# Performance work log

Hardware: AMD Instinct MI355X
Metric: run time of the kernel (lower is better)

## Reference

```python
import jax, jax.numpy as jnp
import numpy as np

VOCAB, EMB, HID, OUT = 50257, 512, 1024, 5
SEQ, BATCH = 512, 64


def setup_inputs() -> dict:
    key = jax.random.key(0)
    ks = jax.random.split(key, 8)
    s_e = 1.0
    s_ih = 1.0 / np.sqrt(HID)
    return {
        "text": jax.random.randint(ks[0], (SEQ, BATCH), 0, VOCAB, dtype=jnp.int32),
        "emb": jax.random.normal(ks[1], (VOCAB, EMB), dtype=jnp.float32) * s_e,
        "W_ih": jax.random.normal(ks[2], (EMB, 3 * HID), dtype=jnp.float32) * s_ih,
        "W_hh": jax.random.normal(ks[3], (HID, 3 * HID), dtype=jnp.float32) * s_ih,
        "b_ih": jax.random.normal(ks[4], (3 * HID,), dtype=jnp.float32) * s_ih,
        "b_hh": jax.random.normal(ks[5], (3 * HID,), dtype=jnp.float32) * s_ih,
        "fc_W": jax.random.normal(ks[6], (HID, OUT), dtype=jnp.float32) * s_ih,
        "fc_b": jnp.zeros((OUT,), dtype=jnp.float32),
    }


def _gru_step(h, x_t, W_ih, W_hh, b_ih, b_hh):
    # Standard GRU cell (torch.nn.GRUCell math):
    # r = sigmoid(x Wir + bir + h Whr + bhr)
    # z = sigmoid(x Wiz + biz + h Whz + bhz)
    # h' = (1 - z) * n + z * h
    gi = x_t @ W_ih + b_ih              # [B, 3H]
    gh = h @ W_hh + b_hh                # [B, 3H]
    i_r, i_z, i_n = jnp.split(gi, 3, axis=-1)
    h_r, h_z, h_n = jnp.split(gh, 3, axis=-1)
    r = jax.nn.sigmoid(i_r + h_r)
    z = jax.nn.sigmoid(i_z + h_z)
    n = jnp.tanh(i_n + r * h_n)
    return (1.0 - z) * n + z * h


def reference(text, emb, W_ih, W_hh, b_ih, b_hh, fc_W, fc_b):
    embedded = emb[text]                # [S, B, E]
    h0 = jnp.zeros((embedded.shape[1], HID), dtype=embedded.dtype)

    def step(h, x_t):
        h_new = _gru_step(h, x_t, W_ih, W_hh, b_ih, b_hh)
        return h_new, None

    h_final, _ = jax.lax.scan(step, h0, embedded)
    return h_final @ fc_W + fc_b        # [B, OUT]
```

## Files before the change

kernel.cpp:

```cpp
#include <hip/hip_runtime.h>
#include <hip/hip_cooperative_groups.h>
#include <hip/hip_bf16.h>
#include <math.h>

constexpr int EMBD  = 512;
constexpr int HID   = 1024;
constexpr int NOUT  = 5;
constexpr int SEQ   = 512;
constexpr int BATCH = 64;

constexpr int NBLK = 64;
constexpr int NTHR = 512;
constexpr int JPB  = 16;

typedef __attribute__((ext_vector_type(8))) short bf16x8;
typedef __attribute__((ext_vector_type(4))) float f32x4;

__device__ inline unsigned short f2bf(float f) {
    __hip_bfloat16 h = __float2bfloat16(f);
    return *reinterpret_cast<unsigned short*>(&h);
}

__device__ inline bf16x8 cvt8v(f32x4 a, f32x4 b) {
    bf16x8 r;
#pragma unroll
    for (int i = 0; i < 4; i++) { __hip_bfloat16 h = __float2bfloat16(a[i]); r[i]     = *reinterpret_cast<short*>(&h); }
#pragma unroll
    for (int i = 0; i < 4; i++) { __hip_bfloat16 h = __float2bfloat16(b[i]); r[4 + i] = *reinterpret_cast<short*>(&h); }
    return r;
}

__device__ inline unsigned long long load_a8(const unsigned short* p) {
    return __hip_atomic_load((const unsigned long long*)p,
                             __ATOMIC_RELAXED, __HIP_MEMORY_SCOPE_AGENT);
}
__device__ inline void store_a8(unsigned short* p, unsigned long long v) {
    __hip_atomic_store((unsigned long long*)p, v,
                       __ATOMIC_RELAXED, __HIP_MEMORY_SCOPE_AGENT);
}
__device__ inline bf16x8 load_frag(const unsigned short* p) {
    union { unsigned long long u[2]; bf16x8 v; } r;
    r.u[0] = load_a8(p);
    r.u[1] = load_a8(p + 4);
    return r.v;
}

__device__ inline float sigm(float x) { return 1.f / (1.f + __expf(-x)); }
__device__ inline float ftanh(float x) { return 1.f - 2.f / (1.f + __expf(2.f * x)); }

__global__ __launch_bounds__(256) void pack_w(const float* __restrict__ W,
                                              unsigned short* __restrict__ out,
                                              int K) {
    const int nkt = K / 32;
    long idx = (long)blockIdx.x * 256 + threadIdx.x;
    const long total = (long)NBLK * 3 * nkt * 64;
    if (idx >= total) return;
    const int lane = idx & 63;
    long rest = idx >> 6;
    const int kt = rest % nkt; rest /= nkt;
    const int nt = rest % 3;
    const int g  = rest / 3;
    const int k0  = kt * 32 + (lane >> 4) * 8;
    const int col = nt * HID + g * JPB + (lane & 15);
    unsigned short* o = out + idx * 8;
#pragma unroll
    for (int i = 0; i < 8; i++)
        o[i] = f2bf(W[(long)(k0 + i) * 3072 + col]);
}

__global__ __launch_bounds__(256) void embed_x(const int* __restrict__ text,
                                               const float* __restrict__ emb,
                                               unsigned short* __restrict__ xfrag) {
    long idx = (long)blockIdx.x * 256 + threadIdx.x;
    if (idx >= (long)SEQ * 4 * 16 * 64) return;
    const int lane = idx & 63;
    const int kt   = (idx >> 6) & 15;
    const int bt   = (idx >> 10) & 3;
    const int t    = (int)(idx >> 12);
    const int b    = bt * 16 + (lane & 15);
    const int e0   = kt * 32 + (lane >> 4) * 8;
    const int tok  = text[t * BATCH + b];
    const float* s = emb + (long)tok * EMBD + e0;
    *(bf16x8*)(xfrag + idx * 8) = cvt8v(*(const f32x4*)s, *(const f32x4*)(s + 4));
}

__global__ void __launch_bounds__(NTHR, 2) gru_mfma(
    const unsigned short* __restrict__ xfrag,
    const float*          __restrict__ b_ih,
    const float*          __restrict__ b_hh,
    const float*          __restrict__ fc_W,
    const float*          __restrict__ fc_b,
    const unsigned short* __restrict__ whh_f,
    const unsigned short* __restrict__ wih_f,
    unsigned short*       __restrict__ hbuf,
    int*                  __restrict__ flags,
    float*                __restrict__ out)
{
    const int g    = blockIdx.x;
    const int tid  = threadIdx.x;
    const int lane = tid & 63;
    const int w    = tid >> 6;
    const int mp   = w >> 2;
    const int kq   = w & 3;
    const int l16  = lane & 15;
    const int lhi  = lane >> 4;

    __shared__ float red[8][8][256];
    __shared__ unsigned short hx[64][20];

    constexpr int HFRAG = 4 * 32 * 64 * 8;

    for (int i = tid; i < 512; i += NTHR)
        store_a8(hbuf + ((long)g * 512 + i) * 4, 0ull);

    const int jg = g * JPB + l16;
    const float bir  = b_ih[jg],           bhr = b_hh[jg];
    const float biz  = b_ih[HID + jg],     bhz = b_hh[HID + jg];
    const float bin_ = b_ih[2 * HID + jg], bhn = b_hh[2 * HID + jg];

    const bool gateW  = (kq < 2);
    const bool storeW = (kq >= 2);
    const int  mtG    = mp * 2 + kq;
    const int  mtS    = mp * 2 + (kq - 2);
    float hp[4] = {0.f, 0.f, 0.f, 0.f};

    bf16x8 xa0[4], xa1[4];
    auto loadX = [&](int t) {
        const unsigned short* base = xfrag + (long)t * (4 * 16 * 64 * 8);
#pragma unroll
        for (int kk = 0; kk < 4; kk++) {
            const int kt = kq * 4 + kk;
            xa0[kk] = load_frag(base + (((2 * mp + 0) * 16 + kt) * 64 + lane) * 8);
            xa1[kk] = load_frag(base + (((2 * mp + 1) * 16 + kt) * 64 + lane) * 8);
        }
    };

    const int sb  = mtS * 16 + ((lane >> 1) & 15);
    const int sjl = ((lane >> 1) >> 4) * 8 + 4 * (lane & 1);
    const long sdst = (((long)mtS * 32 + (g >> 1)) * 64) * 8 + 256 * (g & 1) + lane * 4;

    const unsigned short* whh_g = whh_f + (long)g * 3 * 32 * 64 * 8;
    const unsigned short* wih_g = wih_f + (long)g * 3 * 16 * 64 * 8;

    asm volatile("s_waitcnt vmcnt(0)" ::: "memory");
    __syncthreads();
    if (tid == 0)
        __hip_atomic_store(&flags[g], 1, __ATOMIC_RELAXED, __HIP_MEMORY_SCOPE_AGENT);
    loadX(0);
    if (tid < 64) {
        int f = __hip_atomic_load(&flags[tid], __ATOMIC_RELAXED, __HIP_MEMORY_SCOPE_AGENT);
        while (__any(f < 1)) {
            __builtin_amdgcn_s_sleep(1);
            f = __hip_atomic_load(&flags[tid], __ATOMIC_RELAXED, __HIP_MEMORY_SCOPE_AGENT);
        }
    }
    __syncthreads();

    for (int t = 0; t < SEQ; ++t) {
        const unsigned short* hr = hbuf + (long)(t & 1) * HFRAG;
        unsigned short*       hw = hbuf + (long)((t + 1) & 1) * HFRAG;

        bf16x8 ha0[8], ha1[8];
#pragma unroll
        for (int kk = 0; kk < 8; kk++) {
            const int kt = kq * 8 + kk;
            ha0[kk] = load_frag(hr + (((long)(2 * mp + 0) * 32 + kt) * 64 + lane) * 8);
            ha1[kk] = load_frag(hr + (((long)(2 * mp + 1) * 32 + kt) * 64 + lane) * 8);
        }

        f32x4 aR0 = {0,0,0,0}, aR1 = {0,0,0,0};
        f32x4 aZ0 = {0,0,0,0}, aZ1 = {0,0,0,0};
        f32x4 aGh0 = {0,0,0,0}, aGh1 = {0,0,0,0};
        f32x4 aGi0 = {0,0,0,0}, aGi1 = {0,0,0,0};

#pragma unroll
        for (int kk = 0; kk < 4; kk++) {
            const unsigned short* bp = wih_g + (((long)(kq * 4 + kk)) * 64 + lane) * 8;
            const bf16x8 bR = *(const bf16x8*)(bp);
            const bf16x8 bZ = *(const bf16x8*)(bp + 16 * 64 * 8);
            const bf16x8 bN = *(const bf16x8*)(bp + 2 * 16 * 64 * 8);
            aR0  = __builtin_amdgcn_mfma_f32_16x16x32_bf16(xa0[kk], bR, aR0, 0, 0, 0);
            aR1  = __builtin_amdgcn_mfma_f32_16x16x32_bf16(xa1[kk], bR, aR1, 0, 0, 0);
            aZ0  = __builtin_amdgcn_mfma_f32_16x16x32_bf16(xa0[kk], bZ, aZ0, 0, 0, 0);
            aZ1  = __builtin_amdgcn_mfma_f32_16x16x32_bf16(xa1[kk], bZ, aZ1, 0, 0, 0);
            aGi0 = __builtin_amdgcn_mfma_f32_16x16x32_bf16(xa0[kk], bN, aGi0, 0, 0, 0);
            aGi1 = __builtin_amdgcn_mfma_f32_16x16x32_bf16(xa1[kk], bN, aGi1, 0, 0, 0);
        }

#pragma unroll
        for (int kk = 0; kk < 8; kk++) {
            const int kt = kq * 8 + kk;
            const unsigned short* bp = whh_g + (((long)kt) * 64 + lane) * 8;
            const bf16x8 bR = *(const bf16x8*)(bp);
            const bf16x8 bZ = *(const bf16x8*)(bp + 32 * 64 * 8);
            const bf16x8 bN = *(const bf16x8*)(bp + 2 * 32 * 64 * 8);
            aR0  = __builtin_amdgcn_mfma_f32_16x16x32_bf16(ha0[kk], bR, aR0, 0, 0, 0);
            aR1  = __builtin_amdgcn_mfma_f32_16x16x32_bf16(ha1[kk], bR, aR1, 0, 0, 0);
            aZ0  = __builtin_amdgcn_mfma_f32_16x16x32_bf16(ha0[kk], bZ, aZ0, 0, 0, 0);
            aZ1  = __builtin_amdgcn_mfma_f32_16x16x32_bf16(ha1[kk], bZ, aZ1, 0, 0, 0);
            aGh0 = __builtin_amdgcn_mfma_f32_16x16x32_bf16(ha0[kk], bN, aGh0, 0, 0, 0);
            aGh1 = __builtin_amdgcn_mfma_f32_16x16x32_bf16(ha1[kk], bN, aGh1, 0, 0, 0);
        }

        *(f32x4*)&red[w][0][lane * 4] = aR0;
        *(f32x4*)&red[w][1][lane * 4] = aR1;
        *(f32x4*)&red[w][2][lane * 4] = aZ0;
        *(f32x4*)&red[w][3][lane * 4] = aZ1;
        *(f32x4*)&red[w][4][lane * 4] = aGh0;
        *(f32x4*)&red[w][5][lane * 4] = aGh1;
        *(f32x4*)&red[w][6][lane * 4] = aGi0;
        *(f32x4*)&red[w][7][lane * 4] = aGi1;
        __syncthreads();

        if (gateW) {
            const int s = kq;
            f32x4 R  = {0,0,0,0}, Z = {0,0,0,0}, Gh = {0,0,0,0}, Gi = {0,0,0,0};
#pragma unroll
            for (int q = 0; q < 4; q++) {
                const int src = mp * 4 + q;
                R  += *(const f32x4*)&red[src][0 + s][lane * 4];
                Z  += *(const f32x4*)&red[src][2 + s][lane * 4];
                Gh += *(const f32x4*)&red[src][4 + s][lane * 4];
                Gi += *(const f32x4*)&red[src][6 + s][lane * 4];
            }
#pragma unroll
            for (int r = 0; r < 4; r++) {
                const float rr = sigm(R[r] + bir + bhr);
                const float zz = sigm(Z[r] + biz + bhz);
                const float nn = ftanh(Gi[r] + bin_ + rr * (Gh[r] + bhn));
                const float hn = (1.f - zz) * nn + zz * hp[r];
                hp[r] = hn;
                hx[mtG * 16 + lhi * 4 + r][l16] = f2bf(hn);
            }
        }
        __syncthreads();

        if (storeW) {
            const unsigned long long v =
                *(const unsigned long long*)&hx[sb][sjl];
            store_a8(hw + sdst, v);
            asm volatile("s_waitcnt vmcnt(0)" ::: "memory");
        }
        __syncthreads();

        if (tid == 0)
            __hip_atomic_store(&flags[g], t + 2, __ATOMIC_RELAXED, __HIP_MEMORY_SCOPE_AGENT);
        loadX((t + 1 < SEQ) ? t + 1 : SEQ - 1);
        if (tid < 64) {
            int f = __hip_atomic_load(&flags[tid], __ATOMIC_RELAXED, __HIP_MEMORY_SCOPE_AGENT);
            while (__any(f < t + 2)) {
                __builtin_amdgcn_s_sleep(1);
                f = __hip_atomic_load(&flags[tid], __ATOMIC_RELAXED, __HIP_MEMORY_SCOPE_AGENT);
            }
        }
        __syncthreads();
    }

    float (*hsl)[JPB] = reinterpret_cast<float(*)[JPB]>(&red[0][0][0]);
    if (gateW) {
#pragma unroll
        for (int r = 0; r < 4; r++) {
            const int b = mtG * 16 + lhi * 4 + r;
            hsl[b][l16] = hp[r];
        }
    }
    __syncthreads();
    if (tid < BATCH * NOUT) {
        const int b = tid / NOUT, o = tid - b * NOUT;
        float acc = (g == 0) ? fc_b[o] : 0.0f;
#pragma unroll
        for (int jl = 0; jl < JPB; jl++)
            acc += hsl[b][jl] * fc_W[(g * JPB + jl) * NOUT + o];
        atomicAdd(&out[tid], acc);
    }
}

extern "C" void kernel_launch(void* const* d_in, const int* in_sizes, int n_in,
                              void* d_out, int out_size, void* d_ws, size_t ws_size,
                              hipStream_t stream) {
    const int*   text = (const int*)  d_in[0];
    const float* emb  = (const float*)d_in[1];
    const float* W_ih = (const float*)d_in[2];
    const float* W_hh = (const float*)d_in[3];
    const float* b_ih = (const float*)d_in[4];
    const float* b_hh = (const float*)d_in[5];
    const float* fc_W = (const float*)d_in[6];
    const float* fc_b = (const float*)d_in[7];
    float* out = (float*)d_out;

    char* ws = (char*)d_ws;
    int*            flags = (int*)(ws);
    unsigned short* hbuf  = (unsigned short*)(ws + 4096);
    unsigned short* whh_f = (unsigned short*)(ws + 4096 + 262144);
    unsigned short* wih_f = (unsigned short*)(ws + 4096 + 262144 + 6291456);
    unsigned short* xfrag = (unsigned short*)(ws + 4096 + 262144 + 6291456 + 3145728);

    hipMemsetAsync(flags, 0, 4096, stream);
    hipMemsetAsync(out, 0, (size_t)out_size * sizeof(float), stream);

    const long nfrag_hh = (long)NBLK * 3 * 32 * 64;
    const long nfrag_ih = (long)NBLK * 3 * 16 * 64;
    pack_w<<<(int)((nfrag_hh + 255) / 256), 256, 0, stream>>>(W_hh, whh_f, HID);
    pack_w<<<(int)((nfrag_ih + 255) / 256), 256, 0, stream>>>(W_ih, wih_f, EMBD);

    const long nx = (long)SEQ * 4 * 16 * 64;
    embed_x<<<(int)((nx + 255) / 256), 256, 0, stream>>>(text, emb, xfrag);

    void* args[] = { (void*)&xfrag, (void*)&b_ih, (void*)&b_hh,
                     (void*)&fc_W, (void*)&fc_b, (void*)&whh_f, (void*)&wih_f,
                     (void*)&hbuf, (void*)&flags, (void*)&out };
    hipLaunchCooperativeKernel((void*)gru_mfma, dim3(NBLK), dim3(NTHR), args, 0, stream);
}
```

Measured before the change: 3.001 ms.

## Replace per-step flag barrier with sentinel-tagged 4-slot hidden-state ring

Removes the per-timestep flag store/poll grid barrier and the store waitcnt. Instead, h is written into a 4-slot ring buffer, and readers spin directly on the data until no sentinel values remain. Each writer also re-arms the slot two steps ahead with sentinels. This cuts the barrier round-trip latency on the serial critical path. The risk is a memory-ordering problem: the 8-byte data stores are relaxed, and there is no fence between a sentinel reset and later reads, so correctness relies on per-chunk atomicity and on the ring depth. The x load also moves from prefetch-after-barrier to the start of each step.

```diff
diff --git a/kernel.cpp b/kernel.cpp
--- a/kernel.cpp
+++ b/kernel.cpp
@@ -12,6 +12,9 @@
 constexpr int NBLK = 64;
 constexpr int NTHR = 512;
 constexpr int JPB  = 16;
+constexpr int NS   = 4;
+
+constexpr unsigned long long SENT = 0xFFFFFFFFFFFFFFFFull;
 
 typedef __attribute__((ext_vector_type(8))) short bf16x8;
 typedef __attribute__((ext_vector_type(4))) float f32x4;
@@ -42,6 +45,11 @@
     union { unsigned long long u[2]; bf16x8 v; } r;
     r.u[0] = load_a8(p);
     r.u[1] = load_a8(p + 4);
+    return r.v;
+}
+__device__ inline bf16x8 mkfrag(unsigned long long lo, unsigned long long hi) {
+    union { unsigned long long u[2]; bf16x8 v; } r;
+    r.u[0] = lo; r.u[1] = hi;
     return r.v;
 }
 
@@ -92,7 +100,7 @@
     const float*          __restrict__ fc_b,
     const unsigned short* __restrict__ whh_f,
     const unsigned short* __restrict__ wih_f,
-    unsigned short*       __restrict__ hbuf,
+    unsigned short*       __restrict__ hring,
     int*                  __restrict__ flags,
     float*                __restrict__ out)
 {
@@ -110,8 +118,14 @@
 
     constexpr int HFRAG = 4 * 32 * 64 * 8;
 
-    for (int i = tid; i < 512; i += NTHR)
-        store_a8(hbuf + ((long)g * 512 + i) * 4, 0ull);
+    for (int i = tid; i < 4 * 256; i += NTHR) {
+        const int slot = i >> 8;
+        const int c    = i & 255;
+        const int mt   = c >> 6;
+        const int ln   = c & 63;
+        const long off = (((long)mt * 32 + (g >> 1)) * 64) * 8 + 256 * (g & 1) + ln * 4;
+        store_a8(hring + (long)slot * HFRAG + off, (slot == 3) ? 0ull : SENT);
+    }
 
     const int jg = g * JPB + l16;
     const float bir  = b_ih[jg],           bhr = b_hh[jg];
@@ -146,7 +160,6 @@
     __syncthreads();
     if (tid == 0)
         __hip_atomic_store(&flags[g], 1, __ATOMIC_RELAXED, __HIP_MEMORY_SCOPE_AGENT);
-    loadX(0);
     if (tid < 64) {
         int f = __hip_atomic_load(&flags[tid], __ATOMIC_RELAXED, __HIP_MEMORY_SCOPE_AGENT);
         while (__any(f < 1)) {
@@ -157,15 +170,36 @@
     __syncthreads();
 
     for (int t = 0; t < SEQ; ++t) {
-        const unsigned short* hr = hbuf + (long)(t & 1) * HFRAG;
-        unsigned short*       hw = hbuf + (long)((t + 1) & 1) * HFRAG;
-
+        const unsigned short* hr = hring + (long)((t + 3) & 3) * HFRAG;
+        unsigned short*       hw = hring + (long)(t & 3) * HFRAG;
+        unsigned short*       hs = hring + (long)((t + 2) & 3) * HFRAG;
+
+        loadX(t);
+
+        const unsigned short* p0 = hr + (((long)(2 * mp + 0) * 32 + kq * 8) * 64 + lane) * 8;
+        const unsigned short* p1 = hr + (((long)(2 * mp + 1) * 32 + kq * 8) * 64 + lane) * 8;
+        unsigned long long a0lo[8], a0hi[8], a1lo[8], a1hi[8];
+        while (true) {
+            bool ok = true;
+#pragma unroll
+            for (int kk = 0; kk < 8; kk++) {
+                a0lo[kk] = load_a8(p0 + kk * 512);
+                a0hi[kk] = load_a8(p0 + kk * 512 + 4);
+                a1lo[kk] = load_a8(p1 + kk * 512);
+                a1hi[kk] = load_a8(p1 + kk * 512 + 4);
+            }
+#pragma unroll
+            for (int kk = 0; kk < 8; kk++)
+                ok = ok && (a0lo[kk] != SENT) && (a0hi[kk] != SENT)
+                        && (a1lo[kk] != SENT) && (a1hi[kk] != SENT);
+            if (__all(ok)) break;
+            __builtin_amdgcn_s_sleep(1);
+        }
         bf16x8 ha0[8], ha1[8];
 #pragma unroll
         for (int kk = 0; kk < 8; kk++) {
-            const int kt = kq * 8 + kk;
-            ha0[kk] = load_frag(hr + (((long)(2 * mp + 0) * 32 + kt) * 64 + lane) * 8);
-            ha1[kk] = load_frag(hr + (((long)(2 * mp + 1) * 32 + kt) * 64 + lane) * 8);
+            ha0[kk] = mkfrag(a0lo[kk], a0hi[kk]);
+            ha1[kk] = mkfrag(a1lo[kk], a1hi[kk]);
         }
 
         f32x4 aR0 = {0,0,0,0}, aR1 = {0,0,0,0};
@@ -236,26 +270,13 @@
         __syncthreads();
 
         if (storeW) {
-            const unsigned long long v =
-                *(const unsigned long long*)&hx[sb][sjl];
+            const unsigned long long v = *(const unsigned long long*)&hx[sb][sjl];
             store_a8(hw + sdst, v);
-            asm volatile("s_waitcnt vmcnt(0)" ::: "memory");
-        }
-        __syncthreads();
-
-        if (tid == 0)
-            __hip_atomic_store(&flags[g], t + 2, __ATOMIC_RELAXED, __HIP_MEMORY_SCOPE_AGENT);
-        loadX((t + 1 < SEQ) ? t + 1 : SEQ - 1);
-        if (tid < 64) {
-            int f = __hip_atomic_load(&flags[tid], __ATOMIC_RELAXED, __HIP_MEMORY_SCOPE_AGENT);
-            while (__any(f < t + 2)) {
-                __builtin_amdgcn_s_sleep(1);
-                f = __hip_atomic_load(&flags[tid], __ATOMIC_RELAXED, __HIP_MEMORY_SCOPE_AGENT);
-            }
-        }
-        __syncthreads();
-    }
-
+            store_a8(hs + sdst, SENT);
+        }
+    }
+
+    __syncthreads();
     float (*hsl)[JPB] = reinterpret_cast<float(*)[JPB]>(&red[0][0][0]);
     if (gateW) {
 #pragma unroll
@@ -290,10 +311,10 @@
 
     char* ws = (char*)d_ws;
     int*            flags = (int*)(ws);
-    unsigned short* hbuf  = (unsigned short*)(ws + 4096);
-    unsigned short* whh_f = (unsigned short*)(ws + 4096 + 262144);
-    unsigned short* wih_f = (unsigned short*)(ws + 4096 + 262144 + 6291456);
-    unsigned short* xfrag = (unsigned short*)(ws + 4096 + 262144 + 6291456 + 3145728);
+    unsigned short* hring = (unsigned short*)(ws + 4096);
+    unsigned short* whh_f = (unsigned short*)(ws + 4096 + 524288);
+    unsigned short* wih_f = (unsigned short*)(ws + 4096 + 524288 + 6291456);
+    unsigned short* xfrag = (unsigned short*)(ws + 4096 + 524288 + 6291456 + 3145728);
 
     hipMemsetAsync(flags, 0, 4096, stream);
     hipMemsetAsync(out, 0, (size_t)out_size * sizeof(float), stream);
@@ -308,6 +329,6 @@
 
     void* args[] = { (void*)&xfrag, (void*)&b_ih, (void*)&b_hh,
                      (void*)&fc_W, (void*)&fc_b, (void*)&whh_f, (void*)&wih_f,
-                     (void*)&hbuf, (void*)&flags, (void*)&out };
+                     (void*)&hring, (void*)&flags, (void*)&out };
     hipLaunchCooperativeKernel((void*)gru_mfma, dim3(NBLK), dim3(NTHR), args, 0, stream);
 }
```

After: 4.143 ms. 38.1% more time.

## Use 4-slot hidden-state ring and overlap input projection with flag wait

Applied to the files above, without the earlier changes.

The hidden-state exchange buffer goes from double to a 4-slot ring. Each wave now spin-waits on the 16 producer flags it actually needs, right before loading h, instead of waiting on all 64 blocks followed by a block barrier. The x·W_ih projection for the next step is issued right after the flag store, so it overlaps other blocks finishing the current step. The intent is to remove the global barrier latency from the serial recurrence. The deeper ring guards against a fast block overwriting a slot that slower readers still need, but the per-wave waits make correctness depend on the ring depth and on memory ordering.

```diff
diff --git a/kernel.cpp b/kernel.cpp
--- a/kernel.cpp
+++ b/kernel.cpp
@@ -92,7 +92,7 @@
     const float*          __restrict__ fc_b,
     const unsigned short* __restrict__ whh_f,
     const unsigned short* __restrict__ wih_f,
-    unsigned short*       __restrict__ hbuf,
+    unsigned short*       __restrict__ hring,
     int*                  __restrict__ flags,
     float*                __restrict__ out)
 {
@@ -110,8 +110,16 @@
 
     constexpr int HFRAG = 4 * 32 * 64 * 8;
 
-    for (int i = tid; i < 512; i += NTHR)
-        store_a8(hbuf + ((long)g * 512 + i) * 4, 0ull);
+    for (int i = tid; i < 256; i += NTHR) {
+        const int mt = i >> 6;
+        const int ln = i & 63;
+        const long off = (((long)mt * 32 + (g >> 1)) * 64) * 8 + 256 * (g & 1) + ln * 4;
+        store_a8(hring + (long)3 * HFRAG + off, 0ull);
+    }
+    asm volatile("s_waitcnt vmcnt(0)" ::: "memory");
+    __syncthreads();
+    if (tid == 0)
+        __hip_atomic_store(&flags[g], 1, __ATOMIC_RELAXED, __HIP_MEMORY_SCOPE_AGENT);
 
     const int jg = g * JPB + l16;
     const float bir  = b_ih[jg],           bhr = b_hh[jg];
@@ -142,37 +150,14 @@
     const unsigned short* whh_g = whh_f + (long)g * 3 * 32 * 64 * 8;
     const unsigned short* wih_g = wih_f + (long)g * 3 * 16 * 64 * 8;
 
-    asm volatile("s_waitcnt vmcnt(0)" ::: "memory");
-    __syncthreads();
-    if (tid == 0)
-        __hip_atomic_store(&flags[g], 1, __ATOMIC_RELAXED, __HIP_MEMORY_SCOPE_AGENT);
-    loadX(0);
-    if (tid < 64) {
-        int f = __hip_atomic_load(&flags[tid], __ATOMIC_RELAXED, __HIP_MEMORY_SCOPE_AGENT);
-        while (__any(f < 1)) {
-            __builtin_amdgcn_s_sleep(1);
-            f = __hip_atomic_load(&flags[tid], __ATOMIC_RELAXED, __HIP_MEMORY_SCOPE_AGENT);
-        }
-    }
-    __syncthreads();
-
-    for (int t = 0; t < SEQ; ++t) {
-        const unsigned short* hr = hbuf + (long)(t & 1) * HFRAG;
-        unsigned short*       hw = hbuf + (long)((t + 1) & 1) * HFRAG;
-
-        bf16x8 ha0[8], ha1[8];
-#pragma unroll
-        for (int kk = 0; kk < 8; kk++) {
-            const int kt = kq * 8 + kk;
-            ha0[kk] = load_frag(hr + (((long)(2 * mp + 0) * 32 + kt) * 64 + lane) * 8);
-            ha1[kk] = load_frag(hr + (((long)(2 * mp + 1) * 32 + kt) * 64 + lane) * 8);
-        }
-
-        f32x4 aR0 = {0,0,0,0}, aR1 = {0,0,0,0};
-        f32x4 aZ0 = {0,0,0,0}, aZ1 = {0,0,0,0};
-        f32x4 aGh0 = {0,0,0,0}, aGh1 = {0,0,0,0};
-        f32x4 aGi0 = {0,0,0,0}, aGi1 = {0,0,0,0};
-
+    f32x4 aR0, aR1, aZ0, aZ1, aGh0, aGh1, aGi0, aGi1;
+
+    auto giStep = [&](int t) {
+        loadX(t);
+        aR0 = f32x4{0,0,0,0};  aR1 = f32x4{0,0,0,0};
+        aZ0 = f32x4{0,0,0,0};  aZ1 = f32x4{0,0,0,0};
+        aGh0 = f32x4{0,0,0,0}; aGh1 = f32x4{0,0,0,0};
+        aGi0 = f32x4{0,0,0,0}; aGi1 = f32x4{0,0,0,0};
 #pragma unroll
         for (int kk = 0; kk < 4; kk++) {
             const unsigned short* bp = wih_g + (((long)(kq * 4 + kk)) * 64 + lane) * 8;
@@ -185,6 +170,31 @@
             aZ1  = __builtin_amdgcn_mfma_f32_16x16x32_bf16(xa1[kk], bZ, aZ1, 0, 0, 0);
             aGi0 = __builtin_amdgcn_mfma_f32_16x16x32_bf16(xa0[kk], bN, aGi0, 0, 0, 0);
             aGi1 = __builtin_amdgcn_mfma_f32_16x16x32_bf16(xa1[kk], bN, aGi1, 0, 0, 0);
+        }
+    };
+
+    giStep(0);
+
+    const int fidx = 16 * kq + (lane & 15);
+
+    for (int t = 0; t < SEQ; ++t) {
+        const unsigned short* hr = hring + (long)((t + 3) & 3) * HFRAG;
+        unsigned short*       hw = hring + (long)(t & 3) * HFRAG;
+
+        {
+            int f = __hip_atomic_load(&flags[fidx], __ATOMIC_RELAXED, __HIP_MEMORY_SCOPE_AGENT);
+            while (__any(f < t + 1)) {
+                __builtin_amdgcn_s_sleep(1);
+                f = __hip_atomic_load(&flags[fidx], __ATOMIC_RELAXED, __HIP_MEMORY_SCOPE_AGENT);
+            }
+        }
+
+        bf16x8 ha0[8], ha1[8];
+#pragma unroll
+        for (int kk = 0; kk < 8; kk++) {
+            const int kt = kq * 8 + kk;
+            ha0[kk] = load_frag(hr + (((long)(2 * mp + 0) * 32 + kt) * 64 + lane) * 8);
+            ha1[kk] = load_frag(hr + (((long)(2 * mp + 1) * 32 + kt) * 64 + lane) * 8);
         }
 
 #pragma unroll
@@ -236,8 +246,7 @@
         __syncthreads();
 
         if (storeW) {
-            const unsigned long long v =
-                *(const unsigned long long*)&hx[sb][sjl];
+            const unsigned long long v = *(const unsigned long long*)&hx[sb][sjl];
             store_a8(hw + sdst, v);
             asm volatile("s_waitcnt vmcnt(0)" ::: "memory");
         }
@@ -245,15 +254,7 @@
 
         if (tid == 0)
             __hip_atomic_store(&flags[g], t + 2, __ATOMIC_RELAXED, __HIP_MEMORY_SCOPE_AGENT);
-        loadX((t + 1 < SEQ) ? t + 1 : SEQ - 1);
-        if (tid < 64) {
-            int f = __hip_atomic_load(&flags[tid], __ATOMIC_RELAXED, __HIP_MEMORY_SCOPE_AGENT);
-            while (__any(f < t + 2)) {
-                __builtin_amdgcn_s_sleep(1);
-                f = __hip_atomic_load(&flags[tid], __ATOMIC_RELAXED, __HIP_MEMORY_SCOPE_AGENT);
-            }
-        }
-        __syncthreads();
+        if (t + 1 < SEQ) giStep(t + 1);
     }
 
     float (*hsl)[JPB] = reinterpret_cast<float(*)[JPB]>(&red[0][0][0]);
@@ -290,10 +291,10 @@
 
     char* ws = (char*)d_ws;
     int*            flags = (int*)(ws);
-    unsigned short* hbuf  = (unsigned short*)(ws + 4096);
-    unsigned short* whh_f = (unsigned short*)(ws + 4096 + 262144);
-    unsigned short* wih_f = (unsigned short*)(ws + 4096 + 262144 + 6291456);
-    unsigned short* xfrag = (unsigned short*)(ws + 4096 + 262144 + 6291456 + 3145728);
+    unsigned short* hring = (unsigned short*)(ws + 4096);
+    unsigned short* whh_f = (unsigned short*)(ws + 4096 + 524288);
+    unsigned short* wih_f = (unsigned short*)(ws + 4096 + 524288 + 6291456);
+    unsigned short* xfrag = (unsigned short*)(ws + 4096 + 524288 + 6291456 + 3145728);
 
     hipMemsetAsync(flags, 0, 4096, stream);
     hipMemsetAsync(out, 0, (size_t)out_size * sizeof(float), stream);
@@ -308,6 +309,6 @@
 
     void* args[] = { (void*)&xfrag, (void*)&b_ih, (void*)&b_hh,
                      (void*)&fc_W, (void*)&fc_b, (void*)&whh_f, (void*)&wih_f,
-                     (void*)&hbuf, (void*)&flags, (void*)&out };
+                     (void*)&hring, (void*)&flags, (void*)&out };
     hipLaunchCooperativeKernel((void*)gru_mfma, dim3(NBLK), dim3(NTHR), args, 0, stream);
 }
```

Result: slower. 4.069 ms (+35.6%).
